# Kernel tuning notes

Hardware: AMD Instinct MI355X
Metric: run time of the kernel (lower is better)

The kernel has to match this reference:

```python
import jax, jax.numpy as jnp
import numpy as np

B, N, D, H = 32, 1024, 512, 8
DH = D // H


def setup_inputs() -> dict:
    key = jax.random.key(0)
    ks = jax.random.split(key, 7)
    s = 1.0 / np.sqrt(D)
    return {
        "x": jax.random.normal(ks[0], (B, N, D), dtype=jnp.float32),
        "Wq": jax.random.uniform(ks[1], (D, D), jnp.float32, -s, s),
        "bq": jax.random.uniform(ks[2], (D,), jnp.float32, -s, s),
        "Wk": jax.random.uniform(ks[3], (D, D), jnp.float32, -s, s),
        "bk": jax.random.uniform(ks[4], (D,), jnp.float32, -s, s),
        "Wv": jax.random.uniform(ks[5], (D, D), jnp.float32, -s, s),
        "bv": jax.random.uniform(ks[6], (D,), jnp.float32, -s, s),
    }


def reference(x, Wq, bq, Wk, bk, Wv, bv):
    # Linear projections (torch Linear: y = x @ W.T + b)
    q = x @ Wq.T + bq
    k = x @ Wk.T + bk
    v = x @ Wv.T + bv
    # Faithful to the original: RAW reshape [B,N,D] -> [B,H,N,D/H] (no transpose!)
    q = q.reshape(B, H, N, DH)
    k = k.reshape(B, H, N, DH)
    v = v.reshape(B, H, N, DH)
    # Scaled dot-product attention
    scores = jnp.einsum("bhnd,bhmd->bhnm", q, k) / jnp.sqrt(jnp.float32(DH))
    attn = jax.nn.softmax(scores, axis=-1)
    y = jnp.einsum("bhnm,bhmd->bhnd", attn, v)
    # Faithful to the original: raw reshape [B,H,N,DH] -> [B,N,H*DH]
    return y.reshape(B, N, H * DH)
```

## Files before the change

### kernel.cpp

```cpp
#include <hip/hip_runtime.h>
#include <hip/hip_bf16.h>
#include <stdint.h>

#define AS_G __attribute__((address_space(1)))
#define AS_L __attribute__((address_space(3)))

typedef short bf16x8 __attribute__((ext_vector_type(8)));
typedef float f32x4  __attribute__((ext_vector_type(4)));
typedef float f32x16 __attribute__((ext_vector_type(16)));

constexpr int   M_ROWS = 32768;
constexpr float QSCALE = 0.18033688011112042f;

__device__ __forceinline__ ushort f2bf(float f) {
  union { __hip_bfloat16 h; ushort u; } c;
  c.h = __float2bfloat16(f);
  return c.u;
}
__device__ __forceinline__ uint32_t pack2bf(float lo, float hi) {
  union { __hip_bfloat162 b; uint32_t u; } r;
  r.b.x = __float2bfloat16(lo);
  r.b.y = __float2bfloat16(hi);
  return r.u;
}
__device__ __forceinline__ void gload16(const ushort* g, ushort* l) {
  __builtin_amdgcn_global_load_lds((const AS_G uint32_t*)g, (AS_L uint32_t*)l, 16, 0, 0);
}

__device__ __forceinline__ void cvt8(const float* __restrict__ in,
                                     ushort* __restrict__ out, int i) {
  float4 a = reinterpret_cast<const float4*>(in)[2 * i];
  float4 b = reinterpret_cast<const float4*>(in)[2 * i + 1];
  ushort4 o0 = {f2bf(a.x), f2bf(a.y), f2bf(a.z), f2bf(a.w)};
  ushort4 o1 = {f2bf(b.x), f2bf(b.y), f2bf(b.z), f2bf(b.w)};
  reinterpret_cast<ushort4*>(out)[2 * i]     = o0;
  reinterpret_cast<ushort4*>(out)[2 * i + 1] = o1;
}

__global__ __launch_bounds__(256) void cvt_all_kernel(
    const float* __restrict__ x,  const float* __restrict__ wq,
    const float* __restrict__ wk, const float* __restrict__ wv,
    ushort* __restrict__ xb, ushort* __restrict__ wb) {
  const int b = blockIdx.x, t = threadIdx.x;
  if (b < 2048) {
    const int i0 = b * 256 + t;
#pragma unroll
    for (int rep = 0; rep < 4; ++rep) cvt8(x, xb, i0 + rep * 524288);
  } else {
    const int c = b - 2048, m = c >> 7;
    const float* src = (m == 0) ? wq : (m == 1 ? wk : wv);
    cvt8(src, wb + m * 262144, (c & 127) * 256 + t);
  }
}

__global__ __launch_bounds__(256) void qkv_gemm_kernel(
    const ushort* __restrict__ Xb, const ushort* __restrict__ Wall,
    const float* __restrict__ bq, const float* __restrict__ bk,
    const float* __restrict__ bv,
    ushort* __restrict__ QKV)
{
  __shared__ ushort As[128 * 64];
  __shared__ ushort Bs[128 * 64];

  const int tile = blockIdx.x;
  const int mt  = tile & 255;
  const int cz  = tile >> 8;
  const int mat = cz >> 2;
  const int nt  = cz & 3;

  const ushort* W    = Wall + (size_t)mat * (512 * 512);
  const float*  bias = (mat == 0) ? bq : (mat == 1 ? bk : bv);
  ushort*       Out  = QKV + (size_t)mat * ((size_t)M_ROWS * 512);
  const float   oscale = (mat == 0) ? QSCALE : 1.0f;

  const int m0 = mt * 128, n0 = nt * 128;
  const int t = threadIdx.x, lane = t & 63, wave = t >> 6;
  const int wr = wave >> 1, wc = wave & 1;
  const int l15 = lane & 15, lg = lane >> 4;

  f32x4 acc[4][4];
#pragma unroll
  for (int i = 0; i < 4; i++)
#pragma unroll
    for (int j = 0; j < 4; j++) acc[i][j] = {0.f, 0.f, 0.f, 0.f};

  for (int kt = 0; kt < 8; ++kt) {
    const int k0 = kt * 64;
    __syncthreads();
#pragma unroll
    for (int i = 0; i < 4; ++i) {
      int c = i * 256 + t, row = c >> 3, col8 = (c & 7) * 8;
      gload16(Xb + (size_t)(m0 + row) * 512 + k0 + col8, As + c * 8);
    }
#pragma unroll
    for (int i = 0; i < 4; ++i) {
      int c = i * 256 + t, row = c >> 3, col8 = (c & 7) * 8;
      gload16(W + (size_t)(n0 + row) * 512 + k0 + col8, Bs + c * 8);
    }
    __syncthreads();
#pragma unroll
    for (int ks = 0; ks < 2; ++ks) {
      bf16x8 af[4], bfr[4];
#pragma unroll
      for (int i = 0; i < 4; ++i) {
        af[i]  = *(const bf16x8*)(As + (wr * 64 + i * 16 + l15) * 64 + ks * 32 + lg * 8);
        bfr[i] = *(const bf16x8*)(Bs + (wc * 64 + i * 16 + l15) * 64 + ks * 32 + lg * 8);
      }
#pragma unroll
      for (int i = 0; i < 4; ++i)
#pragma unroll
        for (int j = 0; j < 4; ++j)
          acc[i][j] = __builtin_amdgcn_mfma_f32_16x16x32_bf16(af[i], bfr[j], acc[i][j], 0, 0, 0);
    }
  }
#pragma unroll
  for (int j = 0; j < 4; ++j) {
    const int col = n0 + wc * 64 + j * 16 + l15;
    const float bc = bias[col];
#pragma unroll
    for (int i = 0; i < 4; ++i) {
      const int row0 = m0 + wr * 64 + i * 16 + lg * 4;
#pragma unroll
      for (int r = 0; r < 4; ++r)
        Out[(size_t)(row0 + r) * 512 + col] = f2bf((acc[i][j][r] + bc) * oscale);
    }
  }
}

__global__ __launch_bounds__(256) void vtrans_kernel(
    const ushort* __restrict__ Vn, ushort* __restrict__ VT)
{
  __shared__ ushort T[64][258];
  const int bh = blockIdx.x >> 2, nc = blockIdx.x & 3;
  const ushort* src = Vn + (size_t)bh * 65536 + nc * 16384;
  ushort* dst = VT + (size_t)bh * 65536 + nc * 256;
  const int t = threadIdx.x;
#pragma unroll
  for (int i = 0; i < 8; ++i) {
    int c = i * 256 + t, n = c >> 3, col8 = (c & 7) * 8;
    ushort tmp[8];
    *(int4*)tmp = *(const int4*)(src + n * 64 + col8);
#pragma unroll
    for (int j = 0; j < 8; ++j) T[col8 + j][n] = tmp[j];
  }
  __syncthreads();
#pragma unroll
  for (int i = 0; i < 8; ++i) {
    int c = i * 256 + t, dh = c >> 5, a8 = (c & 31) * 8;
    *(int4*)(dst + (size_t)dh * 1024 + a8) = *(const int4*)(&T[dh][a8]);
  }
}

__global__ __launch_bounds__(256, 4) void attn_kernel(
    const ushort* __restrict__ QKV,
    const ushort* __restrict__ VTg_,
    float* __restrict__ Out)
{
  constexpr int PLANE = M_ROWS * 512;
  __shared__ ushort SMEM[64 * 258];
  ushort* sK = SMEM;
  ushort* sV = SMEM + 8192;
  float* Lbuf = (float*)SMEM;

  const int blk = blockIdx.x;
  const int bh = blk >> 3, qb = blk & 7;
  const ushort* Qg  = QKV + (size_t)bh * 65536;
  const ushort* Kg  = QKV + (size_t)PLANE + (size_t)bh * 65536;
  const ushort* Vtg = VTg_ + (size_t)bh * 65536;

  const int t = threadIdx.x, lane = t & 63, wave = t >> 6;
  const int l31 = lane & 31, h = lane >> 5;
  const int q = qb * 128 + wave * 32 + l31;

  bf16x8 qf[4];
#pragma unroll
  for (int ks = 0; ks < 4; ++ks)
    qf[ks] = *(const bf16x8*)(Qg + (size_t)q * 64 + ks * 16 + h * 8);

  int off[2][4];
#pragma unroll
  for (int tt = 0; tt < 2; ++tt) {
    const int row = tt * 32 + l31;
#pragma unroll
    for (int ks = 0; ks < 4; ++ks)
      off[tt][ks] = row * 64 + (((ks * 2 + h) ^ (row & 7)) << 3);
  }

  float mrow = -1e30f, lrow = 0.f;
  f32x16 o[2];
#pragma unroll
  for (int r = 0; r < 16; ++r) { o[0][r] = 0.f; o[1][r] = 0.f; }

#pragma unroll
  for (int i = 0; i < 2; ++i) {
    int c = i * 256 + t, row = c >> 3, slot = c & 7;
    gload16(Kg + (size_t)row * 64 + ((slot ^ (row & 7)) << 3), sK + c * 8);
    gload16(Vtg + (size_t)row * 1024 + ((slot ^ (row & 7)) << 3), sV + c * 8);
  }
  __syncthreads();

  for (int kv = 0; kv < 16; ++kv) {
    const int cur = kv & 1;
    if (kv < 15) {
      const int nx = cur ^ 1, kn = kv + 1;
#pragma unroll
      for (int i = 0; i < 2; ++i) {
        int c = i * 256 + t, row = c >> 3, slot = c & 7;
        gload16(Kg + (size_t)(kn * 64 + row) * 64 + ((slot ^ (row & 7)) << 3),
                sK + nx * 4096 + c * 8);
        gload16(Vtg + (size_t)row * 1024 + kn * 64 + ((slot ^ (row & 7)) << 3),
                sV + nx * 4096 + c * 8);
      }
    }
    const ushort* Kc = sK + cur * 4096;
    const ushort* Vc = sV + cur * 4096;

    f32x16 st[2];
#pragma unroll
    for (int tt = 0; tt < 2; ++tt) {
      f32x16 a;
#pragma unroll
      for (int r = 0; r < 16; ++r) a[r] = 0.f;
#pragma unroll
      for (int ks = 0; ks < 4; ++ks) {
        bf16x8 kf = *(const bf16x8*)(Kc + off[tt][ks]);
        a = __builtin_amdgcn_mfma_f32_32x32x16_bf16(kf, qf[ks], a, 0, 0, 0);
      }
      st[tt] = a;
    }

    float mx;
    {
      float t8[8];
#pragma unroll
      for (int i = 0; i < 8; ++i)
        t8[i] = fmaxf(fmaxf(st[0][i], st[0][i + 8]), fmaxf(st[1][i], st[1][i + 8]));
      float a0 = fmaxf(fmaxf(t8[0], t8[1]), fmaxf(t8[2], t8[3]));
      float a1 = fmaxf(fmaxf(t8[4], t8[5]), fmaxf(t8[6], t8[7]));
      mx = fmaxf(a0, a1);
    }
    mx = fmaxf(mx, __shfl_xor(mx, 32));
    if (!__all(mx - mrow <= 8.0f)) {
      const float mnew = fmaxf(mrow, mx);
      const float alpha = exp2f(mrow - mnew);
      mrow = mnew;
      lrow *= alpha;
#pragma unroll
      for (int r = 0; r < 16; ++r) { o[0][r] *= alpha; o[1][r] *= alpha; }
    }
#pragma unroll
    for (int tt = 0; tt < 2; ++tt)
#pragma unroll
      for (int r = 0; r < 16; ++r) st[tt][r] = exp2f(st[tt][r] - mrow);
    {
      float s8[8];
#pragma unroll
      for (int i = 0; i < 8; ++i)
        s8[i] = (st[0][i] + st[0][i + 8]) + (st[1][i] + st[1][i + 8]);
      float rs = ((s8[0] + s8[1]) + (s8[2] + s8[3]))
               + ((s8[4] + s8[5]) + (s8[6] + s8[7]));
      rs += __shfl_xor(rs, 32);
      lrow += rs;
    }

#pragma unroll
    for (int tt = 0; tt < 2; ++tt) {
      uint32_t U[8];
#pragma unroll
      for (int p = 0; p < 8; ++p) U[p] = pack2bf(st[tt][2 * p], st[tt][2 * p + 1]);
      uint32_t R[2][2];
#pragma unroll
      for (int s = 0; s < 2; ++s)
#pragma unroll
        for (int i = 0; i < 2; ++i)
          R[s][i] = (uint32_t)__shfl_xor((int)(h ? U[4 * s + i] : U[4 * s + 2 + i]), 32);
#pragma unroll
      for (int s = 0; s < 2; ++s) {
        union { uint32_t u[4]; bf16x8 v; } pf;
        if (h == 0) {
          pf.u[0] = U[4 * s];     pf.u[1] = U[4 * s + 1];
          pf.u[2] = R[s][0];      pf.u[3] = R[s][1];
        } else {
          pf.u[0] = R[s][0];      pf.u[1] = R[s][1];
          pf.u[2] = U[4 * s + 2]; pf.u[3] = U[4 * s + 3];
        }
        const int ks2 = tt * 2 + s;
#pragma unroll
        for (int dt = 0; dt < 2; ++dt) {
          bf16x8 vf = *(const bf16x8*)(Vc + ((ks2 & 1) ? off[dt][2 + (ks2 >> 1)]
                                                       : off[dt][ks2 >> 1]));
          (void)vf;
          bf16x8 vf2 = *(const bf16x8*)(Vc + (dt * 32 + l31) * 64 +
                                        (((ks2 * 2 + h) ^ ((dt * 32 + l31) & 7)) << 3));
          o[dt] = __builtin_amdgcn_mfma_f32_32x32x16_bf16(vf2, pf.v, o[dt], 0, 0, 0);
        }
      }
    }
    __syncthreads();
  }

  const float linv = 1.f / lrow;
#pragma unroll
  for (int dt = 0; dt < 2; ++dt)
#pragma unroll
    for (int r = 0; r < 16; ++r) {
      const int d = dt * 32 + (r & 3) + 8 * (r >> 2) + 4 * h;
      Lbuf[d * 129 + wave * 32 + l31] = o[dt][r] * linv;
    }
  __syncthreads();
  {
    const int qloc = t >> 1, dh = (t & 1) * 32;
    float* ob = Out + (size_t)bh * 65536 + (size_t)(qb * 128 + qloc) * 64 + dh;
#pragma unroll
    for (int c = 0; c < 8; ++c) {
      float4 v = { Lbuf[(dh + 4 * c + 0) * 129 + qloc],
                   Lbuf[(dh + 4 * c + 1) * 129 + qloc],
                   Lbuf[(dh + 4 * c + 2) * 129 + qloc],
                   Lbuf[(dh + 4 * c + 3) * 129 + qloc] };
      *(float4*)(ob + 4 * c) = v;
    }
  }
}

extern "C" void kernel_launch(void* const* d_in, const int* in_sizes, int n_in,
                              void* d_out, int out_size, void* d_ws, size_t ws_size,
                              hipStream_t stream) {
  (void)in_sizes; (void)n_in; (void)out_size; (void)ws_size;
  const float* x  = (const float*)d_in[0];
  const float* Wq = (const float*)d_in[1];
  const float* bq = (const float*)d_in[2];
  const float* Wk = (const float*)d_in[3];
  const float* bk = (const float*)d_in[4];
  const float* Wv = (const float*)d_in[5];
  const float* bv = (const float*)d_in[6];

  ushort* Xb  = (ushort*)d_ws;
  ushort* VT  = (ushort*)d_ws;
  ushort* Wb  = (ushort*)((char*)d_ws + 33554432);
  ushort* QKV = (ushort*)((char*)d_ws + 35127296);
  ushort* Vn  = QKV + 2 * (size_t)M_ROWS * 512;

  cvt_all_kernel<<<2432, 256, 0, stream>>>(x, Wq, Wk, Wv, Xb, Wb);

  qkv_gemm_kernel<<<256 * 12, 256, 0, stream>>>(Xb, Wb, bq, bk, bv, QKV);

  vtrans_kernel<<<1024, 256, 0, stream>>>(Vn, VT);

  attn_kernel<<<256 * 8, 256, 0, stream>>>(QKV, VT, (float*)d_out);
}
```

Before: 248.7 us.

## Pre-permute V^T columns to drop P-fragment cross-lane shuffles; swizzle block order

The V transpose kernel now writes columns in a permuted order matching the MFMA accumulator layout of P. This lets the attention kernel pack P fragments directly from registers, with no __shfl_xor exchanges between half-waves. Row max and sum reductions use permlane32_swap instead of ds_bpermute-based shuffles. The kernel also remaps the block index so the 8 query blocks of one head land on different dispatch slots, and adds s_setprio around the MFMA sections. The layout permutation must stay exactly consistent between the two kernels, or the output will be wrong.

```diff
diff --git a/kernel.cpp b/kernel.cpp
--- a/kernel.cpp
+++ b/kernel.cpp
@@ -8,6 +8,7 @@
 typedef short bf16x8 __attribute__((ext_vector_type(8)));
 typedef float f32x4  __attribute__((ext_vector_type(4)));
 typedef float f32x16 __attribute__((ext_vector_type(16)));
+typedef unsigned int u32x2 __attribute__((ext_vector_type(2)));
 
 constexpr int   M_ROWS = 32768;
 constexpr float QSCALE = 0.18033688011112042f;
@@ -22,6 +23,9 @@
   r.b.x = __float2bfloat16(lo);
   r.b.y = __float2bfloat16(hi);
   return r.u;
+}
+__device__ __forceinline__ u32x2 pswap(uint32_t x) {
+  return __builtin_amdgcn_permlane32_swap(x, x, false, false);
 }
 __device__ __forceinline__ void gload16(const ushort* g, ushort* l) {
   __builtin_amdgcn_global_load_lds((const AS_G uint32_t*)g, (AS_L uint32_t*)l, 16, 0, 0);
@@ -147,7 +151,13 @@
 #pragma unroll
   for (int i = 0; i < 8; ++i) {
     int c = i * 256 + t, dh = c >> 5, a8 = (c & 31) * 8;
-    *(int4*)(dst + (size_t)dh * 1024 + a8) = *(const int4*)(&T[dh][a8]);
+    const int w = a8 & 63;
+    const int pbase = (a8 & 192) + (w >> 5) * 32 + ((w >> 4) & 1) * 16
+                    + ((w >> 3) & 1) * 4;
+    ushort tmp[8];
+    *(uint64_t*)(tmp)     = *(const uint64_t*)(&T[dh][pbase]);
+    *(uint64_t*)(tmp + 4) = *(const uint64_t*)(&T[dh][pbase + 8]);
+    *(int4*)(dst + (size_t)dh * 1024 + a8) = *(const int4*)tmp;
   }
 }
 
@@ -162,7 +172,8 @@
   ushort* sV = SMEM + 8192;
   float* Lbuf = (float*)SMEM;
 
-  const int blk = blockIdx.x;
+  const int raw = blockIdx.x;
+  const int blk = ((raw & 7) << 8) | (raw >> 3);
   const int bh = blk >> 3, qb = blk & 7;
   const ushort* Qg  = QKV + (size_t)bh * 65536;
   const ushort* Kg  = QKV + (size_t)PLANE + (size_t)bh * 65536;
@@ -176,15 +187,6 @@
 #pragma unroll
   for (int ks = 0; ks < 4; ++ks)
     qf[ks] = *(const bf16x8*)(Qg + (size_t)q * 64 + ks * 16 + h * 8);
-
-  int off[2][4];
-#pragma unroll
-  for (int tt = 0; tt < 2; ++tt) {
-    const int row = tt * 32 + l31;
-#pragma unroll
-    for (int ks = 0; ks < 4; ++ks)
-      off[tt][ks] = row * 64 + (((ks * 2 + h) ^ (row & 7)) << 3);
-  }
 
   float mrow = -1e30f, lrow = 0.f;
   f32x16 o[2];
@@ -221,11 +223,14 @@
       f32x16 a;
 #pragma unroll
       for (int r = 0; r < 16; ++r) a[r] = 0.f;
+      __builtin_amdgcn_s_setprio(1);
 #pragma unroll
       for (int ks = 0; ks < 4; ++ks) {
-        bf16x8 kf = *(const bf16x8*)(Kc + off[tt][ks]);
+        const int krow = tt * 32 + l31;
+        bf16x8 kf = *(const bf16x8*)(Kc + krow * 64 + (((ks * 2 + h) ^ (krow & 7)) << 3));
         a = __builtin_amdgcn_mfma_f32_32x32x16_bf16(kf, qf[ks], a, 0, 0, 0);
       }
+      __builtin_amdgcn_s_setprio(0);
       st[tt] = a;
     }
 
@@ -239,7 +244,10 @@
       float a1 = fmaxf(fmaxf(t8[4], t8[5]), fmaxf(t8[6], t8[7]));
       mx = fmaxf(a0, a1);
     }
-    mx = fmaxf(mx, __shfl_xor(mx, 32));
+    {
+      u32x2 d = pswap(__float_as_uint(mx));
+      mx = fmaxf(__uint_as_float(d.x), __uint_as_float(d.y));
+    }
     if (!__all(mx - mrow <= 8.0f)) {
       const float mnew = fmaxf(mrow, mx);
       const float alpha = exp2f(mrow - mnew);
@@ -259,41 +267,28 @@
         s8[i] = (st[0][i] + st[0][i + 8]) + (st[1][i] + st[1][i + 8]);
       float rs = ((s8[0] + s8[1]) + (s8[2] + s8[3]))
                + ((s8[4] + s8[5]) + (s8[6] + s8[7]));
-      rs += __shfl_xor(rs, 32);
-      lrow += rs;
+      u32x2 d = pswap(__float_as_uint(rs));
+      lrow += __uint_as_float(d.x) + __uint_as_float(d.y);
     }
 
 #pragma unroll
     for (int tt = 0; tt < 2; ++tt) {
-      uint32_t U[8];
-#pragma unroll
-      for (int p = 0; p < 8; ++p) U[p] = pack2bf(st[tt][2 * p], st[tt][2 * p + 1]);
-      uint32_t R[2][2];
-#pragma unroll
-      for (int s = 0; s < 2; ++s)
-#pragma unroll
-        for (int i = 0; i < 2; ++i)
-          R[s][i] = (uint32_t)__shfl_xor((int)(h ? U[4 * s + i] : U[4 * s + 2 + i]), 32);
 #pragma unroll
       for (int s = 0; s < 2; ++s) {
         union { uint32_t u[4]; bf16x8 v; } pf;
-        if (h == 0) {
-          pf.u[0] = U[4 * s];     pf.u[1] = U[4 * s + 1];
-          pf.u[2] = R[s][0];      pf.u[3] = R[s][1];
-        } else {
-          pf.u[0] = R[s][0];      pf.u[1] = R[s][1];
-          pf.u[2] = U[4 * s + 2]; pf.u[3] = U[4 * s + 3];
+#pragma unroll
+        for (int i = 0; i < 4; ++i)
+          pf.u[i] = pack2bf(st[tt][8 * s + 2 * i], st[tt][8 * s + 2 * i + 1]);
+        const int ks2 = tt * 2 + s;
+        __builtin_amdgcn_s_setprio(1);
+#pragma unroll
+        for (int dt = 0; dt < 2; ++dt) {
+          const int drow = dt * 32 + l31;
+          bf16x8 vf = *(const bf16x8*)(Vc + drow * 64 +
+                                       (((ks2 * 2 + h) ^ (drow & 7)) << 3));
+          o[dt] = __builtin_amdgcn_mfma_f32_32x32x16_bf16(vf, pf.v, o[dt], 0, 0, 0);
         }
-        const int ks2 = tt * 2 + s;
-#pragma unroll
-        for (int dt = 0; dt < 2; ++dt) {
-          bf16x8 vf = *(const bf16x8*)(Vc + ((ks2 & 1) ? off[dt][2 + (ks2 >> 1)]
-                                                       : off[dt][ks2 >> 1]));
-          (void)vf;
-          bf16x8 vf2 = *(const bf16x8*)(Vc + (dt * 32 + l31) * 64 +
-                                        (((ks2 * 2 + h) ^ ((dt * 32 + l31) & 7)) << 3));
-          o[dt] = __builtin_amdgcn_mfma_f32_32x32x16_bf16(vf2, pf.v, o[dt], 0, 0, 0);
-        }
+        __builtin_amdgcn_s_setprio(0);
       }
     }
     __syncthreads();
```

Measured after the change: 235.6 us. -5.3%, faster.
